# Kernel tuning notes

Measured on AMD Instinct MI355X. Metric: run time of the kernel, lower is better.

## Reference

```python
import jax, jax.numpy as jnp
import numpy as np
import math

N = 8192
D = 512

def setup_inputs() -> dict:
    key = jax.random.key(0)
    k1, k2, k3, k4, k5 = jax.random.split(key, 5)
    x = jax.random.normal(k1, (N, D), dtype=jnp.float32)
    mask = jax.random.randint(k2, (N, N), 0, 2) == 1
    s = 1.0 / math.sqrt(D)
    Wq = jax.random.normal(k3, (D, D), dtype=jnp.float32) * s
    Wk = jax.random.normal(k4, (D, D), dtype=jnp.float32) * s
    Wv = jax.random.normal(k5, (D, D), dtype=jnp.float32) * s
    return {"x": x, "mask": mask, "Wq": Wq, "Wk": Wk, "Wv": Wv}

def reference(x, mask, Wq, Wk, Wv):
    d_model = x.shape[-1]
    # torch nn.Linear: y = x @ W^T
    Q = x @ Wq.T
    K = x @ Wk.T
    V = x @ Wv.T
    scores = (Q @ K.T) / jnp.sqrt(jnp.asarray(d_model, x.dtype))  # [N, N]
    scores = jnp.where(mask, jnp.asarray(-1e9, x.dtype), scores)
    # manual stable softmax, matching the original op sequence
    scores = jnp.exp(scores - jnp.max(scores, axis=1, keepdims=True))
    attn = scores / jnp.sum(scores, axis=-1, keepdims=True)
    cntx = attn @ V
    return (cntx, attn)
```

## Files before the change

### kernel.cpp

```cpp
#include <hip/hip_runtime.h>

#define NTOK 8192
#define DMODEL 512

typedef _Float16 f16;
typedef _Float16 f16x4 __attribute__((ext_vector_type(4)));
typedef _Float16 f16x8 __attribute__((ext_vector_type(8)));
typedef float f32x4 __attribute__((ext_vector_type(4)));

__device__ __forceinline__ void async_ld16(const void* g, void* l) {
  __builtin_amdgcn_global_load_lds((const __attribute__((address_space(1))) void*)g,
                                   (__attribute__((address_space(3))) void*)l, 16, 0, 0);
}

__global__ void pack_f16(const float* __restrict__ s, f16* __restrict__ d, int n) {
  int i = (blockIdx.x * 256 + threadIdx.x) * 4;
  if (i >= n) return;
  float4 v = *(const float4*)(s + i);
  f16x4 h; h.x = (f16)v.x; h.y = (f16)v.y; h.z = (f16)v.z; h.w = (f16)v.w;
  *(f16x4*)(d + i) = h;
}

__global__ __launch_bounds__(256) void transpose_f16(const f16* __restrict__ src,
                                                     f16* __restrict__ dst) {
  __shared__ f16 T[64][72];
  int t = threadIdx.x;
  int tok0 = blockIdx.x * 64, d0 = blockIdx.y * 64;
#pragma unroll
  for (int i = 0; i < 2; ++i) {
    int row = (t >> 3) + i * 32;
    int col = (t & 7) * 8;
    f16x8 v = *(const f16x8*)(src + (size_t)(tok0 + row) * DMODEL + d0 + col);
    *(f16x8*)(&T[row][col]) = v;
  }
  __syncthreads();
#pragma unroll
  for (int i = 0; i < 2; ++i) {
    int od = (t >> 3) + i * 32;
    int ot = (t & 7) * 8;
    f16x8 v;
#pragma unroll
    for (int j = 0; j < 8; ++j) v[j] = T[ot + j][od];
    *(f16x8*)(dst + (size_t)(d0 + od) * NTOK + tok0 + ot) = v;
  }
}

__device__ __forceinline__ void stage128x32(const f16* G, int r0, int k0, int rs,
                                            f16* lds, int t) {
  int wv = t >> 6;
  const f16* g0 = G + (size_t)(r0 + (t >> 2)) * rs + k0 + (t & 3) * 8;
  async_ld16(g0, (char*)lds + wv * 1024);
  const f16* g1 = g0 + (size_t)64 * rs;
  async_ld16(g1, (char*)lds + 4096 + wv * 1024);
}

__global__ __launch_bounds__(256) void qkv_gemm(const f16* __restrict__ X,
                                                const f16* __restrict__ Wall,
                                                f16* __restrict__ Out) {
  __shared__ f16 As[128 * 32];
  __shared__ f16 Bs[128 * 32];
  int t = threadIdx.x;
  int z = blockIdx.z;
  const f16* B = Wall + (size_t)z * DMODEL * DMODEL;
  f16* C = Out + (size_t)z * NTOK * DMODEL;
  int m0 = blockIdx.y * 128, n0 = blockIdx.x * 128;
  int lane = t & 63, wv = t >> 6, quad = lane >> 4, l15 = lane & 15;
  int m_off = (wv & 1) * 64, n_off = (wv >> 1) * 64;
  f32x4 acc[4][4] = {};
  for (int kt = 0; kt < DMODEL; kt += 32) {
    __syncthreads();
    stage128x32(X, m0, kt, DMODEL, As, t);
    stage128x32(B, n0, kt, DMODEL, Bs, t);
    __syncthreads();
    f16x8 af[4], bf[4];
    const f16x8* Av = (const f16x8*)As;
    const f16x8* Bv = (const f16x8*)Bs;
#pragma unroll
    for (int mt = 0; mt < 4; ++mt) af[mt] = Av[(m_off + mt * 16 + l15) * 4 + quad];
#pragma unroll
    for (int nt = 0; nt < 4; ++nt) bf[nt] = Bv[(n_off + nt * 16 + l15) * 4 + quad];
#pragma unroll
    for (int mt = 0; mt < 4; ++mt)
#pragma unroll
      for (int nt = 0; nt < 4; ++nt)
        acc[mt][nt] = __builtin_amdgcn_mfma_f32_16x16x32_f16(af[mt], bf[nt], acc[mt][nt], 0, 0, 0);
  }
#pragma unroll
  for (int mt = 0; mt < 4; ++mt)
#pragma unroll
    for (int nt = 0; nt < 4; ++nt)
#pragma unroll
      for (int r = 0; r < 4; ++r) {
        int row = m0 + m_off + mt * 16 + quad * 4 + r;
        int col = n0 + n_off + nt * 16 + l15;
        C[(size_t)row * DMODEL + col] = (f16)acc[mt][nt][r];
      }
}

__global__ __launch_bounds__(256) void scores_kernel(const f16* __restrict__ Q,
                                                     const f16* __restrict__ Kh,
                                                     const int* __restrict__ mask,
                                                     float* __restrict__ E,
                                                     float* __restrict__ rowsum) {
  __shared__ f16 As[128 * 32];
  __shared__ f16 Bs[128 * 32];
  int t = threadIdx.x;
  int m0 = blockIdx.y * 128, n0 = blockIdx.x * 128;
  int lane = t & 63, wv = t >> 6, quad = lane >> 4, l15 = lane & 15;
  int m_off = (wv & 1) * 64, n_off = (wv >> 1) * 64;
  f32x4 acc[4][4] = {};
  for (int kt = 0; kt < DMODEL; kt += 32) {
    __syncthreads();
    stage128x32(Q, m0, kt, DMODEL, As, t);
    stage128x32(Kh, n0, kt, DMODEL, Bs, t);
    __syncthreads();
    f16x8 af[4], bf[4];
    const f16x8* Av = (const f16x8*)As;
    const f16x8* Bv = (const f16x8*)Bs;
#pragma unroll
    for (int mt = 0; mt < 4; ++mt) af[mt] = Av[(m_off + mt * 16 + l15) * 4 + quad];
#pragma unroll
    for (int nt = 0; nt < 4; ++nt) bf[nt] = Bv[(n_off + nt * 16 + l15) * 4 + quad];
#pragma unroll
    for (int mt = 0; mt < 4; ++mt)
#pragma unroll
      for (int nt = 0; nt < 4; ++nt)
        acc[mt][nt] = __builtin_amdgcn_mfma_f32_16x16x32_f16(af[mt], bf[nt], acc[mt][nt], 0, 0, 0);
  }
  const float scale = 0.044194173824159216f;
#pragma unroll
  for (int mt = 0; mt < 4; ++mt)
#pragma unroll
    for (int r = 0; r < 4; ++r) {
      int row = m0 + m_off + mt * 16 + quad * 4 + r;
      float rs = 0.f;
#pragma unroll
      for (int nt = 0; nt < 4; ++nt) {
        int col = n0 + n_off + nt * 16 + l15;
        size_t idx = (size_t)row * NTOK + col;
        float s = acc[mt][nt][r] * scale;
        float e = mask[idx] ? 0.f : __expf(s);
        E[idx] = e;
        rs += e;
      }
      rs += __shfl_xor(rs, 1);
      rs += __shfl_xor(rs, 2);
      rs += __shfl_xor(rs, 4);
      rs += __shfl_xor(rs, 8);
      if (l15 == 0) atomicAdd(&rowsum[row], rs);
    }
}

__global__ __launch_bounds__(512, 2) void norm_ev(float* __restrict__ E,
                                                  const float* __restrict__ rowsum,
                                                  const f16* __restrict__ Vt,
                                                  float* __restrict__ cntx) {
  __shared__ f16 Es[128 * 32];
  __shared__ f16 Vs[512 * 32];
  int t = threadIdx.x;
  int r0 = blockIdx.x * 128;
  int k0 = blockIdx.y * 2048;
  int lane = t & 63, wv = t >> 6, quad = lane >> 4, l15 = lane & 15;
  int m_off = (wv & 1) * 64, n_off = (wv >> 1) * 128;
  int srow = t >> 3, scol = (t & 7) * 4;
  float rinv0 = 1.f / rowsum[r0 + srow];
  float rinv1 = 1.f / rowsum[r0 + srow + 64];
  f32x4 acc[4][8] = {};
  for (int kt = k0; kt < k0 + 2048; kt += 32) {
    __syncthreads();
    {
      size_t g = (size_t)(r0 + srow) * NTOK + kt + scol;
      float4 v = *(const float4*)(E + g);
      v.x *= rinv0; v.y *= rinv0; v.z *= rinv0; v.w *= rinv0;
      *(float4*)(E + g) = v;
      f16x4 h; h.x = (f16)v.x; h.y = (f16)v.y; h.z = (f16)v.z; h.w = (f16)v.w;
      *(f16x4*)(Es + srow * 32 + scol) = h;
      size_t g2 = g + (size_t)64 * NTOK;
      float4 v2 = *(const float4*)(E + g2);
      v2.x *= rinv1; v2.y *= rinv1; v2.z *= rinv1; v2.w *= rinv1;
      *(float4*)(E + g2) = v2;
      f16x4 h2; h2.x = (f16)v2.x; h2.y = (f16)v2.y; h2.z = (f16)v2.z; h2.w = (f16)v2.w;
      *(f16x4*)(Es + (srow + 64) * 32 + scol) = h2;
    }
#pragma unroll
    for (int i = 0; i < 4; ++i) {
      const f16* g = Vt + (size_t)((i * 512 + t) >> 2) * NTOK + kt + (t & 3) * 8;
      async_ld16(g, (char*)Vs + i * 8192 + wv * 1024);
    }
    __syncthreads();
    f16x8 af[4], bf[8];
    const f16x8* Ev = (const f16x8*)Es;
    const f16x8* Vv = (const f16x8*)Vs;
#pragma unroll
    for (int mt = 0; mt < 4; ++mt) af[mt] = Ev[(m_off + mt * 16 + l15) * 4 + quad];
#pragma unroll
    for (int nt = 0; nt < 8; ++nt) bf[nt] = Vv[(n_off + nt * 16 + l15) * 4 + quad];
#pragma unroll
    for (int mt = 0; mt < 4; ++mt)
#pragma unroll
      for (int nt = 0; nt < 8; ++nt)
        acc[mt][nt] = __builtin_amdgcn_mfma_f32_16x16x32_f16(af[mt], bf[nt], acc[mt][nt], 0, 0, 0);
  }
#pragma unroll
  for (int mt = 0; mt < 4; ++mt)
#pragma unroll
    for (int nt = 0; nt < 8; ++nt)
#pragma unroll
      for (int r = 0; r < 4; ++r) {
        int row = r0 + m_off + mt * 16 + quad * 4 + r;
        int col = n_off + nt * 16 + l15;
        atomicAdd(&cntx[(size_t)row * DMODEL + col], acc[mt][nt][r]);
      }
}

extern "C" void kernel_launch(void* const* d_in, const int* in_sizes, int n_in,
                              void* d_out, int out_size, void* d_ws, size_t ws_size,
                              hipStream_t stream) {
  const float* x  = (const float*)d_in[0];
  const int* mask = (const int*)d_in[1];
  const float* Wq = (const float*)d_in[2];
  const float* Wk = (const float*)d_in[3];
  const float* Wv = (const float*)d_in[4];
  float* cntx = (float*)d_out;
  float* attn = (float*)d_out + (size_t)NTOK * DMODEL;

  f16* xh = (f16*)d_ws;
  f16* Wh = xh + (size_t)NTOK * DMODEL;
  f16* QKV = Wh + (size_t)3 * DMODEL * DMODEL;
  f16* Qh = QKV;
  f16* Kh = QKV + (size_t)NTOK * DMODEL;
  f16* Vh = QKV + (size_t)2 * NTOK * DMODEL;
  f16* Vt = QKV + (size_t)3 * NTOK * DMODEL;
  float* rowsum = (float*)(Vt + (size_t)NTOK * DMODEL);

  hipMemsetAsync(cntx, 0, (size_t)NTOK * DMODEL * sizeof(float), stream);
  hipMemsetAsync(rowsum, 0, NTOK * sizeof(float), stream);

  pack_f16<<<dim3(NTOK * DMODEL / 1024), 256, 0, stream>>>(x, xh, NTOK * DMODEL);
  pack_f16<<<dim3(DMODEL * DMODEL / 1024), 256, 0, stream>>>(Wq, Wh, DMODEL * DMODEL);
  pack_f16<<<dim3(DMODEL * DMODEL / 1024), 256, 0, stream>>>(Wk, Wh + DMODEL * DMODEL, DMODEL * DMODEL);
  pack_f16<<<dim3(DMODEL * DMODEL / 1024), 256, 0, stream>>>(Wv, Wh + 2 * DMODEL * DMODEL, DMODEL * DMODEL);

  qkv_gemm<<<dim3(DMODEL / 128, NTOK / 128, 3), 256, 0, stream>>>(xh, Wh, QKV);
  transpose_f16<<<dim3(NTOK / 64, DMODEL / 64), 256, 0, stream>>>(Vh, Vt);
  scores_kernel<<<dim3(NTOK / 128, NTOK / 128), 256, 0, stream>>>(Qh, Kh, mask, attn, rowsum);
  norm_ev<<<dim3(NTOK / 128, 4), 512, 0, stream>>>(attn, rowsum, Vt, cntx);
}
```

Before: 796.3 us.

## Store unnormalized exp scores as fp16 scratch and write normalized attn once

```diff
diff --git a/kernel.cpp b/kernel.cpp
--- a/kernel.cpp
+++ b/kernel.cpp
@@ -100,7 +100,7 @@
 __global__ __launch_bounds__(256) void scores_kernel(const f16* __restrict__ Q,
                                                      const f16* __restrict__ Kh,
                                                      const int* __restrict__ mask,
-                                                     float* __restrict__ E,
+                                                     f16* __restrict__ E,
                                                      float* __restrict__ rowsum) {
   __shared__ f16 As[128 * 32];
   __shared__ f16 Bs[128 * 32];
@@ -140,7 +140,7 @@
         size_t idx = (size_t)row * NTOK + col;
         float s = acc[mt][nt][r] * scale;
         float e = mask[idx] ? 0.f : __expf(s);
-        E[idx] = e;
+        E[idx] = (f16)e;
         rs += e;
       }
       rs += __shfl_xor(rs, 1);
@@ -151,36 +151,37 @@
     }
 }
 
-__global__ __launch_bounds__(512, 2) void norm_ev(float* __restrict__ E,
+__global__ __launch_bounds__(512, 2) void ev_norm(const f16* __restrict__ E,
                                                   const float* __restrict__ rowsum,
                                                   const f16* __restrict__ Vt,
+                                                  float* __restrict__ attn,
                                                   float* __restrict__ cntx) {
   __shared__ f16 Es[128 * 32];
   __shared__ f16 Vs[512 * 32];
   int t = threadIdx.x;
   int r0 = blockIdx.x * 128;
-  int k0 = blockIdx.y * 2048;
+  int k0 = blockIdx.y * 1024;
   int lane = t & 63, wv = t >> 6, quad = lane >> 4, l15 = lane & 15;
   int m_off = (wv & 1) * 64, n_off = (wv >> 1) * 128;
-  int srow = t >> 3, scol = (t & 7) * 4;
-  float rinv0 = 1.f / rowsum[r0 + srow];
-  float rinv1 = 1.f / rowsum[r0 + srow + 64];
+  int srow = t >> 2, scol = (t & 3) * 8;
+  float rinv = 1.f / rowsum[r0 + srow];
   f32x4 acc[4][8] = {};
-  for (int kt = k0; kt < k0 + 2048; kt += 32) {
+  for (int kt = k0; kt < k0 + 1024; kt += 32) {
     __syncthreads();
     {
       size_t g = (size_t)(r0 + srow) * NTOK + kt + scol;
-      float4 v = *(const float4*)(E + g);
-      v.x *= rinv0; v.y *= rinv0; v.z *= rinv0; v.w *= rinv0;
-      *(float4*)(E + g) = v;
-      f16x4 h; h.x = (f16)v.x; h.y = (f16)v.y; h.z = (f16)v.z; h.w = (f16)v.w;
-      *(f16x4*)(Es + srow * 32 + scol) = h;
-      size_t g2 = g + (size_t)64 * NTOK;
-      float4 v2 = *(const float4*)(E + g2);
-      v2.x *= rinv1; v2.y *= rinv1; v2.z *= rinv1; v2.w *= rinv1;
-      *(float4*)(E + g2) = v2;
-      f16x4 h2; h2.x = (f16)v2.x; h2.y = (f16)v2.y; h2.z = (f16)v2.z; h2.w = (f16)v2.w;
-      *(f16x4*)(Es + (srow + 64) * 32 + scol) = h2;
+      f16x8 e = *(const f16x8*)(E + g);
+      float a[8];
+#pragma unroll
+      for (int j = 0; j < 8; ++j) a[j] = (float)e[j] * rinv;
+      float4 w0 = {a[0], a[1], a[2], a[3]};
+      float4 w1 = {a[4], a[5], a[6], a[7]};
+      *(float4*)(attn + g) = w0;
+      *(float4*)(attn + g + 4) = w1;
+      f16x8 h;
+#pragma unroll
+      for (int j = 0; j < 8; ++j) h[j] = (f16)a[j];
+      *(f16x8*)(Es + srow * 32 + scol) = h;
     }
 #pragma unroll
     for (int i = 0; i < 4; ++i) {
@@ -224,13 +225,14 @@
   float* cntx = (float*)d_out;
   float* attn = (float*)d_out + (size_t)NTOK * DMODEL;
 
-  f16* xh = (f16*)d_ws;
-  f16* Wh = xh + (size_t)NTOK * DMODEL;
-  f16* QKV = Wh + (size_t)3 * DMODEL * DMODEL;
-  f16* Qh = QKV;
-  f16* Kh = QKV + (size_t)NTOK * DMODEL;
-  f16* Vh = QKV + (size_t)2 * NTOK * DMODEL;
-  f16* Vt = QKV + (size_t)3 * NTOK * DMODEL;
+  f16* e16 = (f16*)d_ws;
+  f16* xh  = e16;
+  f16* Wh  = e16 + (size_t)NTOK * DMODEL;
+  f16* QKV = e16 + (size_t)NTOK * NTOK;
+  f16* Qh  = QKV;
+  f16* Kh  = QKV + (size_t)NTOK * DMODEL;
+  f16* Vh  = QKV + (size_t)2 * NTOK * DMODEL;
+  f16* Vt  = QKV + (size_t)3 * NTOK * DMODEL;
   float* rowsum = (float*)(Vt + (size_t)NTOK * DMODEL);
 
   hipMemsetAsync(cntx, 0, (size_t)NTOK * DMODEL * sizeof(float), stream);
@@ -243,6 +245,6 @@
 
   qkv_gemm<<<dim3(DMODEL / 128, NTOK / 128, 3), 256, 0, stream>>>(xh, Wh, QKV);
   transpose_f16<<<dim3(NTOK / 64, DMODEL / 64), 256, 0, stream>>>(Vh, Vt);
-  scores_kernel<<<dim3(NTOK / 128, NTOK / 128), 256, 0, stream>>>(Qh, Kh, mask, attn, rowsum);
-  norm_ev<<<dim3(NTOK / 128, 4), 512, 0, stream>>>(attn, rowsum, Vt, cntx);
-}
+  scores_kernel<<<dim3(NTOK / 128, NTOK / 128), 256, 0, stream>>>(Qh, Kh, mask, e16, rowsum);
+  ev_norm<<<dim3(NTOK / 128, 8), 512, 0, stream>>>(e16, rowsum, Vt, attn, cntx);
+}
```

After: 838.3 us. 5.3% more time.
